# Optimization experiments

Measured on AMD Instinct MI355X. Metric: run time of the kernel, lower is better.

The kernel has to match this reference:

```python
import jax, jax.numpy as jnp
import numpy as np

D_IN = 1024
D_OUT = 1024


def setup_inputs() -> dict:
    key = jax.random.key(0)
    k_x, k_q, k_k, k_v = jax.random.split(key, 4)
    x = jax.random.normal(k_x, (8, 2048, D_IN), dtype=jnp.float32)
    s = 1.0 / np.sqrt(D_IN)
    W_query = jax.random.uniform(k_q, (D_IN, D_OUT), jnp.float32, -s, s)
    W_key = jax.random.uniform(k_k, (D_IN, D_OUT), jnp.float32, -s, s)
    W_value = jax.random.uniform(k_v, (D_IN, D_OUT), jnp.float32, -s, s)
    return {"x": x, "W_query": W_query, "W_key": W_key, "W_value": W_value}


def reference(x, W_query, W_key, W_value):
    # x: [B, N, d_in]; weights stored as [d_in, d_out] (already transposed vs torch Linear)
    B, N, _ = x.shape
    q = x @ W_query          # [B, N, d_out]
    k = x @ W_key
    v = x @ W_value
    scores = jnp.einsum('bnd,bmd->bnm', q, k)  # [B, N, N]
    causal = jnp.tril(jnp.ones((N, N), dtype=bool))
    scores = jnp.where(causal, scores, -jnp.inf)
    weights = jax.nn.softmax(scores / np.sqrt(D_OUT), axis=-1)
    # dropout p=0.0 -> identity
    return jnp.einsum('bnm,bmd->bnd', weights, v)
```

## Files before the change

### kernel.cpp

```cpp
#include <hip/hip_runtime.h>
#include <hip/hip_bf16.h>

typedef unsigned short u16;
typedef unsigned int u32;
typedef __bf16 bf16x8 __attribute__((ext_vector_type(8)));
typedef float f32x4 __attribute__((ext_vector_type(4)));
typedef unsigned int u32x4 __attribute__((ext_vector_type(4)));

#define BATCH 8
#define SEQ   2048
#define DIM   1024
#define M_TOT (BATCH * SEQ)
#define N_QKV (3 * DIM)

#define OFF_QKV  ((size_t)0)
#define OFF_VT   ((size_t)100663296)
#define OFF_C    ((size_t)134217728)
#define OFF_XB   OFF_C
#define OFF_WT   (OFF_C + (size_t)33554432)
#define OFF_S    OFF_C

#define TILE_ELEMS (128 * 64)

__device__ __forceinline__ u16 f32_to_bf16(float f) {
    u32 u = __builtin_bit_cast(u32, f);
    u = (u + 0x7fffu + ((u >> 16) & 1u)) >> 16;
    return (u16)u;
}

__device__ __forceinline__ float bf16_to_f32(u16 h) {
    u32 u = ((u32)h) << 16;
    return __builtin_bit_cast(float, u);
}

__device__ __forceinline__ bf16x8 lds_load8(const u16* p) {
    return __builtin_bit_cast(bf16x8, *(const u32x4*)p);
}

__device__ __forceinline__ void stage_tile64(const u16* gA, size_t lda, u16* ldsA, int tid) {
    int wv = tid >> 6;
#pragma unroll
    for (int iss = 0; iss < 4; ++iss) {
        int s = iss * 256 + tid;
        int row = s >> 3;
        int kg = (s & 7) ^ (row & 7);
        const u16* gp = gA + (size_t)row * lda + (kg << 3);
        u16* lp = ldsA + (size_t)(iss * 256 + wv * 64) * 8;
        __builtin_amdgcn_global_load_lds((const __attribute__((address_space(1))) void*)gp,
                                         (__attribute__((address_space(3))) void*)lp,
                                         16, 0, 0);
    }
}

__device__ __forceinline__ void mfma_step64(const u16* ldsA, const u16* ldsB, int tid,
                                            f32x4 acc[4][4]) {
    int lane = tid & 63;
    int wv = tid >> 6;
    int wr = (wv >> 1) * 64, wc = (wv & 1) * 64;
    int lrow = lane & 15, kgl = lane >> 4;
    int xr = lrow & 7;
#pragma unroll
    for (int ks = 0; ks < 2; ++ks) {
        int off = ((ks * 4 + kgl) ^ xr) << 3;
        bf16x8 a[4], b[4];
#pragma unroll
        for (int i = 0; i < 4; ++i) {
            a[i] = lds_load8(&ldsA[(wr + i * 16 + lrow) * 64 + off]);
            b[i] = lds_load8(&ldsB[(wc + i * 16 + lrow) * 64 + off]);
        }
#pragma unroll
        for (int i = 0; i < 4; ++i)
#pragma unroll
            for (int j = 0; j < 4; ++j)
                acc[i][j] = __builtin_amdgcn_mfma_f32_16x16x32_bf16(a[i], b[j], acc[i][j], 0, 0, 0);
    }
}

__device__ __forceinline__ void gemm_loop_db(const u16* __restrict__ A, size_t lda,
                                             const u16* __restrict__ B, size_t ldb,
                                             int KT, u16* ldsA, u16* ldsB, int tid,
                                             f32x4 acc[4][4]) {
    stage_tile64(A, lda, ldsA, tid);
    stage_tile64(B, ldb, ldsB, tid);
    int cur = 0;
    for (int t = 0; t < KT; ++t) {
        int nxt = cur ^ 1;
        if (t + 1 < KT) {
            stage_tile64(A + (size_t)(t + 1) * 64, lda, ldsA + nxt * TILE_ELEMS, tid);
            stage_tile64(B + (size_t)(t + 1) * 64, ldb, ldsB + nxt * TILE_ELEMS, tid);
            asm volatile("s_waitcnt vmcnt(8)" ::: "memory");
        } else {
            asm volatile("s_waitcnt vmcnt(0)" ::: "memory");
        }
        __builtin_amdgcn_s_barrier();
        __builtin_amdgcn_sched_barrier(0);
        mfma_step64(ldsA + cur * TILE_ELEMS, ldsB + cur * TILE_ELEMS, tid, acc);
        __builtin_amdgcn_s_barrier();
        __builtin_amdgcn_sched_barrier(0);
        cur = nxt;
    }
}

__global__ __launch_bounds__(256) void cast_x_kernel(const float* __restrict__ x,
                                                     u16* __restrict__ xb) {
    size_t g = (size_t)blockIdx.x * 256 + threadIdx.x;
    f32x4 v = ((const f32x4*)x)[g];
    u16 o[4] = {f32_to_bf16(v.x), f32_to_bf16(v.y), f32_to_bf16(v.z), f32_to_bf16(v.w)};
    *(unsigned long long*)(xb + g * 4) = *(const unsigned long long*)o;
}

__global__ __launch_bounds__(256) void transpose_w_kernel(const float* __restrict__ wq,
                                                          const float* __restrict__ wk,
                                                          const float* __restrict__ wv,
                                                          u16* __restrict__ wt) {
    __shared__ __align__(16) u16 tile[64][80];
    const float* w = blockIdx.z == 0 ? wq : (blockIdx.z == 1 ? wk : wv);
    int k0 = blockIdx.x * 64, n0 = blockIdx.y * 64;
    for (int g = threadIdx.x; g < 1024; g += 256) {
        int r = g >> 4, c = (g & 15) << 2;
        f32x4 v = *(const f32x4*)(w + (size_t)(k0 + r) * 1024 + n0 + c);
        tile[r][c + 0] = f32_to_bf16(v.x);
        tile[r][c + 1] = f32_to_bf16(v.y);
        tile[r][c + 2] = f32_to_bf16(v.z);
        tile[r][c + 3] = f32_to_bf16(v.w);
    }
    __syncthreads();
    u16* out = wt + (size_t)blockIdx.z * 1024 * 1024;
    for (int g = threadIdx.x; g < 512; g += 256) {
        int nr = g >> 3, kc = (g & 7) << 3;
        __align__(16) u16 tmp[8];
#pragma unroll
        for (int i = 0; i < 8; ++i) tmp[i] = tile[kc + i][nr];
        *(u32x4*)(out + (size_t)(n0 + nr) * 1024 + k0 + kc) = *(const u32x4*)tmp;
    }
}

__global__ __launch_bounds__(256, 2) void gemm_qkv_kernel(const u16* __restrict__ xb,
                                                          const u16* __restrict__ wt,
                                                          u16* __restrict__ qkv) {
    __shared__ __align__(16) u16 ldsA[2 * TILE_ELEMS];
    __shared__ __align__(16) u16 ldsB[2 * TILE_ELEMS];
    int nt = blockIdx.x, mt = blockIdx.y;
    const u16* A = xb + (size_t)mt * 128 * 1024;
    const u16* B = wt + (size_t)nt * 128 * 1024;
    int tid = threadIdx.x;
    f32x4 acc[4][4] = {};
    gemm_loop_db(A, 1024, B, 1024, 16, ldsA, ldsB, tid, acc);
    int lane = tid & 63, wv = tid >> 6;
    int wr = (wv >> 1) * 64, wc = (wv & 1) * 64;
    int r0 = (lane >> 4) * 4, c0 = lane & 15;
    size_t mbase = (size_t)mt * 128;
    int nbase = nt * 128;
#pragma unroll
    for (int i = 0; i < 4; ++i)
#pragma unroll
        for (int j = 0; j < 4; ++j) {
            int col = nbase + wc + j * 16 + c0;
            float scale = (col < 1024) ? 0.03125f : 1.0f;
#pragma unroll
            for (int r = 0; r < 4; ++r) {
                int row = wr + i * 16 + r0 + r;
                qkv[(mbase + row) * (size_t)N_QKV + col] = f32_to_bf16(acc[i][j][r] * scale);
            }
        }
}

__global__ __launch_bounds__(256) void transpose_v_kernel(const u16* __restrict__ qkv,
                                                          u16* __restrict__ vt) {
    __shared__ __align__(16) u16 tile[64][80];
    int m0 = blockIdx.x * 64, d0 = blockIdx.y * 64, b = blockIdx.z;
    const u16* src = qkv + (size_t)b * SEQ * N_QKV + 2048;
    for (int g = threadIdx.x; g < 512; g += 256) {
        int r = g >> 3, c = (g & 7) << 3;
        *(u32x4*)&tile[r][c] = *(const u32x4*)(src + (size_t)(m0 + r) * N_QKV + d0 + c);
    }
    __syncthreads();
    u16* dst = vt + (size_t)b * DIM * SEQ;
    for (int g = threadIdx.x; g < 512; g += 256) {
        int dr = g >> 3, mc = (g & 7) << 3;
        __align__(16) u16 tmp[8];
#pragma unroll
        for (int i = 0; i < 8; ++i) tmp[i] = tile[mc + i][dr];
        *(u32x4*)(dst + (size_t)(d0 + dr) * SEQ + m0 + mc) = *(const u32x4*)tmp;
    }
}

__global__ __launch_bounds__(256, 2) void gemm_scores_kernel(const u16* __restrict__ qkv,
                                                             u16* __restrict__ S) {
    int t = blockIdx.x;
    int b = blockIdx.y;
    int ntile = 0;
#pragma unroll
    for (int it = 1; it < 16; ++it)
        if ((it * (it + 1)) / 2 <= t) ntile = it;
    int mtile = t - (ntile * (ntile + 1)) / 2;
    __shared__ __align__(16) u16 ldsA[2 * TILE_ELEMS];
    __shared__ __align__(16) u16 ldsB[2 * TILE_ELEMS];
    const u16* A = qkv + (size_t)b * SEQ * N_QKV + (size_t)ntile * 128 * N_QKV;
    const u16* B = qkv + (size_t)b * SEQ * N_QKV + (size_t)mtile * 128 * N_QKV + 1024;
    int tid = threadIdx.x;
    f32x4 acc[4][4] = {};
    gemm_loop_db(A, N_QKV, B, N_QKV, 16, ldsA, ldsB, tid, acc);
    u16* out = S + (size_t)b * SEQ * SEQ + (size_t)ntile * 128 * SEQ + (size_t)mtile * 128;
    int lane = tid & 63, wv = tid >> 6;
    int wr = (wv >> 1) * 64, wc = (wv & 1) * 64;
    int r0 = (lane >> 4) * 4, c0 = lane & 15;
#pragma unroll
    for (int i = 0; i < 4; ++i)
#pragma unroll
        for (int j = 0; j < 4; ++j) {
            int col = wc + j * 16 + c0;
#pragma unroll
            for (int r = 0; r < 4; ++r) {
                int row = wr + i * 16 + r0 + r;
                out[(size_t)row * SEQ + col] = f32_to_bf16(acc[i][j][r]);
            }
        }
}

__global__ __launch_bounds__(256) void softmax_kernel(u16* __restrict__ SP) {
    int gr = blockIdx.x;
    int n = gr & 2047;
    u16* s = SP + (size_t)gr * SEQ;
    __shared__ float red[4];
    int t = threadIdx.x;
    int base = t << 3;
    int len = n + 1;
    float v[8];
    float lmax = -3.0e38f;
    if (base < len) {
        u32x4 raw = *(const u32x4*)(s + base);
        const u16* h = (const u16*)&raw;
#pragma unroll
        for (int i = 0; i < 8; ++i) {
            v[i] = (base + i < len) ? bf16_to_f32(h[i]) : -3.0e38f;
            lmax = fmaxf(lmax, v[i]);
        }
    } else {
#pragma unroll
        for (int i = 0; i < 8; ++i) v[i] = -3.0e38f;
    }
#pragma unroll
    for (int off = 32; off; off >>= 1) lmax = fmaxf(lmax, __shfl_xor(lmax, off, 64));
    if ((t & 63) == 0) red[t >> 6] = lmax;
    __syncthreads();
    float gmax = fmaxf(fmaxf(red[0], red[1]), fmaxf(red[2], red[3]));
    __syncthreads();
    float lsum = 0.f;
#pragma unroll
    for (int i = 0; i < 8; ++i) {
        float e = __expf(v[i] - gmax);
        v[i] = e;
        lsum += e;
    }
#pragma unroll
    for (int off = 32; off; off >>= 1) lsum += __shfl_xor(lsum, off, 64);
    if ((t & 63) == 0) red[t >> 6] = lsum;
    __syncthreads();
    float inv = 1.0f / (red[0] + red[1] + red[2] + red[3]);
    __align__(16) u16 o[8];
#pragma unroll
    for (int i = 0; i < 8; ++i) o[i] = f32_to_bf16(v[i] * inv);
    *(u32x4*)(s + base) = *(const u32x4*)o;
}

__global__ __launch_bounds__(256, 2) void gemm_out_kernel(const u16* __restrict__ P,
                                                          const u16* __restrict__ vt,
                                                          float* __restrict__ O) {
    __shared__ __align__(16) u16 ldsA[2 * TILE_ELEMS];
    __shared__ __align__(16) u16 ldsB[2 * TILE_ELEMS];
    int dt = blockIdx.x, b = blockIdx.z;
    int ntile = (SEQ / 128 - 1) - blockIdx.y;
    const u16* A = P + (size_t)b * SEQ * SEQ + (size_t)ntile * 128 * SEQ;
    const u16* B = vt + (size_t)b * DIM * SEQ + (size_t)dt * 128 * SEQ;
    int tid = threadIdx.x;
    f32x4 acc[4][4] = {};
    int kTiles = ntile * 2 + 2;
    gemm_loop_db(A, SEQ, B, SEQ, kTiles, ldsA, ldsB, tid, acc);
    float* out = O + (size_t)b * SEQ * DIM + (size_t)ntile * 128 * DIM + (size_t)dt * 128;
    int lane = tid & 63, wv = tid >> 6;
    int wr = (wv >> 1) * 64, wc = (wv & 1) * 64;
    int r0 = (lane >> 4) * 4, c0 = lane & 15;
#pragma unroll
    for (int i = 0; i < 4; ++i)
#pragma unroll
        for (int j = 0; j < 4; ++j) {
            int col = wc + j * 16 + c0;
#pragma unroll
            for (int r = 0; r < 4; ++r) {
                int row = wr + i * 16 + r0 + r;
                out[(size_t)row * DIM + col] = acc[i][j][r];
            }
        }
}

extern "C" void kernel_launch(void* const* d_in, const int* in_sizes, int n_in,
                              void* d_out, int out_size, void* d_ws, size_t ws_size,
                              hipStream_t stream) {
    const float* x = (const float*)d_in[0];
    const float* wq = (const float*)d_in[1];
    const float* wk = (const float*)d_in[2];
    const float* wv = (const float*)d_in[3];
    char* ws = (char*)d_ws;
    u16* qkv = (u16*)(ws + OFF_QKV);
    u16* vt = (u16*)(ws + OFF_VT);
    u16* xb = (u16*)(ws + OFF_XB);
    u16* wt = (u16*)(ws + OFF_WT);
    u16* S = (u16*)(ws + OFF_S);
    float* O = (float*)d_out;

    cast_x_kernel<<<M_TOT * DIM / 4 / 256, 256, 0, stream>>>(x, xb);
    transpose_w_kernel<<<dim3(16, 16, 3), 256, 0, stream>>>(wq, wk, wv, wt);
    gemm_qkv_kernel<<<dim3(N_QKV / 128, M_TOT / 128), 256, 0, stream>>>(xb, wt, qkv);
    transpose_v_kernel<<<dim3(SEQ / 64, DIM / 64, BATCH), 256, 0, stream>>>(qkv, vt);
    gemm_scores_kernel<<<dim3(136, BATCH), 256, 0, stream>>>(qkv, S);
    softmax_kernel<<<BATCH * SEQ, 256, 0, stream>>>(S);
    gemm_out_kernel<<<dim3(DIM / 128, SEQ / 128, BATCH), 256, 0, stream>>>(S, vt, O);
}
```

Before: 409.3 us.

## Load GEMM B operand directly from global into registers, drop LDS double buffering

```diff
diff --git a/kernel.cpp b/kernel.cpp
--- a/kernel.cpp
+++ b/kernel.cpp
@@ -34,6 +34,10 @@
 }
 
 __device__ __forceinline__ bf16x8 lds_load8(const u16* p) {
+    return __builtin_bit_cast(bf16x8, *(const u32x4*)p);
+}
+
+__device__ __forceinline__ bf16x8 gload8(const u16* __restrict__ p) {
     return __builtin_bit_cast(bf16x8, *(const u32x4*)p);
 }
 
@@ -52,52 +56,45 @@
     }
 }
 
-__device__ __forceinline__ void mfma_step64(const u16* ldsA, const u16* ldsB, int tid,
-                                            f32x4 acc[4][4]) {
+__device__ __forceinline__ void mfma_step_bd(const u16* ldsA, const u16* __restrict__ Bg,
+                                             size_t ldb, int tid, f32x4 acc[4][4]) {
     int lane = tid & 63;
     int wv = tid >> 6;
     int wr = (wv >> 1) * 64, wc = (wv & 1) * 64;
     int lrow = lane & 15, kgl = lane >> 4;
     int xr = lrow & 7;
+    bf16x8 b0[4], b1[4];
+#pragma unroll
+    for (int j = 0; j < 4; ++j) {
+        const u16* bp = Bg + (size_t)(wc + j * 16 + lrow) * ldb + kgl * 8;
+        b0[j] = gload8(bp);
+        b1[j] = gload8(bp + 32);
+    }
 #pragma unroll
     for (int ks = 0; ks < 2; ++ks) {
         int off = ((ks * 4 + kgl) ^ xr) << 3;
-        bf16x8 a[4], b[4];
-#pragma unroll
-        for (int i = 0; i < 4; ++i) {
+        bf16x8 a[4];
+#pragma unroll
+        for (int i = 0; i < 4; ++i)
             a[i] = lds_load8(&ldsA[(wr + i * 16 + lrow) * 64 + off]);
-            b[i] = lds_load8(&ldsB[(wc + i * 16 + lrow) * 64 + off]);
-        }
 #pragma unroll
         for (int i = 0; i < 4; ++i)
 #pragma unroll
             for (int j = 0; j < 4; ++j)
-                acc[i][j] = __builtin_amdgcn_mfma_f32_16x16x32_bf16(a[i], b[j], acc[i][j], 0, 0, 0);
-    }
-}
-
-__device__ __forceinline__ void gemm_loop_db(const u16* __restrict__ A, size_t lda,
+                acc[i][j] = __builtin_amdgcn_mfma_f32_16x16x32_bf16(
+                    a[i], ks ? b1[j] : b0[j], acc[i][j], 0, 0, 0);
+    }
+}
+
+__device__ __forceinline__ void gemm_loop_bd(const u16* __restrict__ A, size_t lda,
                                              const u16* __restrict__ B, size_t ldb,
-                                             int KT, u16* ldsA, u16* ldsB, int tid,
+                                             int KT, u16* ldsA, int tid,
                                              f32x4 acc[4][4]) {
-    stage_tile64(A, lda, ldsA, tid);
-    stage_tile64(B, ldb, ldsB, tid);
-    int cur = 0;
-    for (int t = 0; t < KT; ++t) {
-        int nxt = cur ^ 1;
-        if (t + 1 < KT) {
-            stage_tile64(A + (size_t)(t + 1) * 64, lda, ldsA + nxt * TILE_ELEMS, tid);
-            stage_tile64(B + (size_t)(t + 1) * 64, ldb, ldsB + nxt * TILE_ELEMS, tid);
-            asm volatile("s_waitcnt vmcnt(8)" ::: "memory");
-        } else {
-            asm volatile("s_waitcnt vmcnt(0)" ::: "memory");
-        }
-        __builtin_amdgcn_s_barrier();
-        __builtin_amdgcn_sched_barrier(0);
-        mfma_step64(ldsA + cur * TILE_ELEMS, ldsB + cur * TILE_ELEMS, tid, acc);
-        __builtin_amdgcn_s_barrier();
-        __builtin_amdgcn_sched_barrier(0);
-        cur = nxt;
+    for (int kt = 0; kt < KT; ++kt) {
+        __syncthreads();
+        stage_tile64(A + (size_t)kt * 64, lda, ldsA, tid);
+        __syncthreads();
+        mfma_step_bd(ldsA, B + (size_t)kt * 64, ldb, tid, acc);
     }
 }
 
@@ -138,14 +135,13 @@
 __global__ __launch_bounds__(256, 2) void gemm_qkv_kernel(const u16* __restrict__ xb,
                                                           const u16* __restrict__ wt,
                                                           u16* __restrict__ qkv) {
-    __shared__ __align__(16) u16 ldsA[2 * TILE_ELEMS];
-    __shared__ __align__(16) u16 ldsB[2 * TILE_ELEMS];
+    __shared__ __align__(16) u16 ldsA[TILE_ELEMS];
     int nt = blockIdx.x, mt = blockIdx.y;
     const u16* A = xb + (size_t)mt * 128 * 1024;
     const u16* B = wt + (size_t)nt * 128 * 1024;
     int tid = threadIdx.x;
     f32x4 acc[4][4] = {};
-    gemm_loop_db(A, 1024, B, 1024, 16, ldsA, ldsB, tid, acc);
+    gemm_loop_bd(A, 1024, B, 1024, 16, ldsA, tid, acc);
     int lane = tid & 63, wv = tid >> 6;
     int wr = (wv >> 1) * 64, wc = (wv & 1) * 64;
     int r0 = (lane >> 4) * 4, c0 = lane & 15;
@@ -194,13 +190,12 @@
     for (int it = 1; it < 16; ++it)
         if ((it * (it + 1)) / 2 <= t) ntile = it;
     int mtile = t - (ntile * (ntile + 1)) / 2;
-    __shared__ __align__(16) u16 ldsA[2 * TILE_ELEMS];
-    __shared__ __align__(16) u16 ldsB[2 * TILE_ELEMS];
+    __shared__ __align__(16) u16 ldsA[TILE_ELEMS];
     const u16* A = qkv + (size_t)b * SEQ * N_QKV + (size_t)ntile * 128 * N_QKV;
     const u16* B = qkv + (size_t)b * SEQ * N_QKV + (size_t)mtile * 128 * N_QKV + 1024;
     int tid = threadIdx.x;
     f32x4 acc[4][4] = {};
-    gemm_loop_db(A, N_QKV, B, N_QKV, 16, ldsA, ldsB, tid, acc);
+    gemm_loop_bd(A, N_QKV, B, N_QKV, 16, ldsA, tid, acc);
     u16* out = S + (size_t)b * SEQ * SEQ + (size_t)ntile * 128 * SEQ + (size_t)mtile * 128;
     int lane = tid & 63, wv = tid >> 6;
     int wr = (wv >> 1) * 64, wc = (wv & 1) * 64;
@@ -267,8 +262,7 @@
 __global__ __launch_bounds__(256, 2) void gemm_out_kernel(const u16* __restrict__ P,
                                                           const u16* __restrict__ vt,
                                                           float* __restrict__ O) {
-    __shared__ __align__(16) u16 ldsA[2 * TILE_ELEMS];
-    __shared__ __align__(16) u16 ldsB[2 * TILE_ELEMS];
+    __shared__ __align__(16) u16 ldsA[TILE_ELEMS];
     int dt = blockIdx.x, b = blockIdx.z;
     int ntile = (SEQ / 128 - 1) - blockIdx.y;
     const u16* A = P + (size_t)b * SEQ * SEQ + (size_t)ntile * 128 * SEQ;
@@ -276,7 +270,7 @@
     int tid = threadIdx.x;
     f32x4 acc[4][4] = {};
     int kTiles = ntile * 2 + 2;
-    gemm_loop_db(A, SEQ, B, SEQ, kTiles, ldsA, ldsB, tid, acc);
+    gemm_loop_bd(A, SEQ, B, SEQ, kTiles, ldsA, tid, acc);
     float* out = O + (size_t)b * SEQ * DIM + (size_t)ntile * 128 * DIM + (size_t)dt * 128;
     int lane = tid & 63, wv = tid >> 6;
     int wr = (wv >> 1) * 64, wc = (wv & 1) * 64;
```

Result: slower. 604.6 us (+47.7%).
